# Optimization experiments

Hardware: AMD Instinct MI355X
Metric: run time of the kernel (lower is better)

## Reference

```python
import jax, jax.numpy as jnp
import numpy as np

B, S, E, H = 2, 2048, 1024, 16
HD = E // H


def setup_inputs() -> dict:
    key = jax.random.key(0)
    ks = jax.random.split(key, 5)
    scale = 1.0 / np.sqrt(E)
    return {
        "query": jax.random.normal(ks[0], (B, S, E), jnp.float32),
        "key": jax.random.normal(ks[1], (B, S, E), jnp.float32),
        "value": jax.random.normal(ks[2], (B, S, E), jnp.float32),
        "qkv_w": jax.random.normal(ks[3], (3 * E, E), jnp.float32) * scale,
        "qkv_b": jnp.zeros((3 * E,), jnp.float32),
        "out_w": jax.random.normal(ks[4], (E, E), jnp.float32) * scale,
        "out_b": jnp.zeros((E,), jnp.float32),
    }


def reference(query, key, value, qkv_w, qkv_b, out_w, out_b):
    # Fused QKV projection from query (module ignores key/value contents)
    qkv = query @ qkv_w.T + qkv_b                      # [B,S,3E]
    qkv = qkv.reshape(B, S, 3, H, HD)
    q = qkv[:, :, 0].transpose(0, 2, 1, 3)             # [B,H,S,HD]
    k = qkv[:, :, 1].transpose(0, 2, 1, 3)
    v = qkv[:, :, 2].transpose(0, 2, 1, 3)
    scaling = 1.0 / np.sqrt(HD)
    scores = jnp.einsum("bhqd,bhkd->bhqk", q, k) * scaling  # [B,H,S,S]
    probs = jax.nn.softmax(scores, axis=-1)
    ctx = jnp.einsum("bhqk,bhkd->bhqd", probs, v)      # [B,H,S,HD]
    ctx = ctx.transpose(0, 2, 1, 3).reshape(B, S, E)
    return ctx @ out_w.T + out_b
```

## Files before the change

### kernel.cpp

```cpp
#include <hip/hip_runtime.h>
#include <hip/hip_bf16.h>
#include <math.h>

#define BB 2
#define SS 2048
#define EE 1024
#define HH 16
#define HD 64

typedef __bf16 bf16;
typedef __bf16 bf16x8 __attribute__((ext_vector_type(8)));
typedef float floatx4 __attribute__((ext_vector_type(4)));
typedef float floatx16 __attribute__((ext_vector_type(16)));

#define MFMA(a, b, c) __builtin_amdgcn_mfma_f32_16x16x32_bf16(a, b, c, 0, 0, 0)
#define MFMA32(a, b, c) __builtin_amdgcn_mfma_f32_32x32x16_bf16(a, b, c, 0, 0, 0)

__device__ inline void async16(const bf16* g, bf16* l) {
    __builtin_amdgcn_global_load_lds(
        (const __attribute__((address_space(1))) void*)g,
        (__attribute__((address_space(3))) void*)l, 16, 0, 0);
}

__device__ inline unsigned cvt_pk_bf16(float a, float b) {
    unsigned r;
    asm("v_cvt_pk_bf16_f32 %0, %1, %2" : "=v"(r) : "v"(a), "v"(b));
    return r;
}

__global__ __launch_bounds__(256) void cvt3(
    const float* __restrict__ a, const float* __restrict__ b,
    const float* __restrict__ c,
    bf16* __restrict__ oa, bf16* __restrict__ ob, bf16* __restrict__ oc) {
    const long NA = (long)4096 * 1024, NB = (long)3072 * 1024, NC = (long)1024 * 1024;
    const long total = (NA + NB + NC) >> 2;
    long i = (long)blockIdx.x * blockDim.x + threadIdx.x;
    const long stride = (long)gridDim.x * blockDim.x;
    for (; i < total; i += stride) {
        const long e = i << 2;
        const float* src;
        bf16* dst;
        if (e < NA)           { src = a + e;            dst = oa + e; }
        else if (e < NA + NB) { src = b + (e - NA);     dst = ob + (e - NA); }
        else                  { src = c + (e - NA - NB); dst = oc + (e - NA - NB); }
        float4 v = *(const float4*)src;
        union { bf16 h[4]; uint2 u; } t;
        t.h[0] = (bf16)v.x; t.h[1] = (bf16)v.y; t.h[2] = (bf16)v.z; t.h[3] = (bf16)v.w;
        *(uint2*)dst = t.u;
    }
}

__global__ __launch_bounds__(256) void qkv_gemm(
    const bf16* __restrict__ A, const bf16* __restrict__ W,
    const float* __restrict__ bias,
    bf16* __restrict__ Qw, bf16* __restrict__ Kw, bf16* __restrict__ Vtw) {
    __shared__ __align__(16) bf16 As[128 * 64];
    __shared__ __align__(16) bf16 Bs[128 * 64];
    const int tid  = threadIdx.x;
    const int wave = tid >> 6, lane = tid & 63;
    const int quad = lane >> 4, l16 = lane & 15;
    const int wr = wave >> 1, wc = wave & 1;
    const int m0 = blockIdx.y * 128, n0 = blockIdx.x * 128;
    const int lr = lane >> 3;
    const int lc = (lane & 7) * 8;

    const bf16* Ag = A + (long)(m0 + wave * 32 + lr) * 1024 + lc;
    const bf16* Bg = W + (long)(n0 + wave * 32 + lr) * 1024 + lc;
    bf16* Al = As + (wave * 32) * 64 + lane * 8;
    bf16* Bl = Bs + (wave * 32) * 64 + lane * 8;

    floatx4 acc[4][4] = {};

    for (int k0 = 0; k0 < 1024; k0 += 64) {
        __syncthreads();
#pragma unroll
        for (int j = 0; j < 4; ++j) {
            async16(Ag + (long)j * 8 * 1024 + k0, Al + j * 8 * 64);
            async16(Bg + (long)j * 8 * 1024 + k0, Bl + j * 8 * 64);
        }
        __syncthreads();
#pragma unroll
        for (int c = 0; c < 2; ++c) {
            bf16x8 af[4], bfr[4];
#pragma unroll
            for (int mi = 0; mi < 4; ++mi)
                af[mi] = *(const bf16x8*)&As[(wr * 64 + mi * 16 + l16) * 64 + c * 32 + quad * 8];
#pragma unroll
            for (int ni = 0; ni < 4; ++ni)
                bfr[ni] = *(const bf16x8*)&Bs[(wc * 64 + ni * 16 + l16) * 64 + c * 32 + quad * 8];
#pragma unroll
            for (int mi = 0; mi < 4; ++mi)
#pragma unroll
                for (int ni = 0; ni < 4; ++ni)
                    acc[mi][ni] = MFMA(af[mi], bfr[ni], acc[mi][ni]);
        }
    }

#pragma unroll
    for (int mi = 0; mi < 4; ++mi)
#pragma unroll
        for (int ni = 0; ni < 4; ++ni) {
            const int n = n0 + wc * 64 + ni * 16 + l16;
            const float bn = bias[n];
            const int sel = n >> 10;
            const int e = n & 1023, h = e >> 6, d = e & 63;
            if (sel == 2) {
                const int m_base = m0 + wr * 64 + mi * 16 + quad * 4;
                const int b = m_base >> 11, s0 = m_base & 2047;
                union { bf16 h4[4]; uint2 u; } t;
#pragma unroll
                for (int r = 0; r < 4; ++r)
                    t.h4[r] = (bf16)(acc[mi][ni][r] + bn);
                *(uint2*)&Vtw[((long)(b * HH + h) * HD + d) * SS + s0] = t.u;
            } else {
#pragma unroll
                for (int r = 0; r < 4; ++r) {
                    const int m = m0 + wr * 64 + mi * 16 + quad * 4 + r;
                    const int b = m >> 11, s = m & 2047;
                    const float v = acc[mi][ni][r] + bn;
                    if (sel == 0)
                        Qw[((long)(b * HH + h) * SS + s) * HD + d] = (bf16)(v * 0.125f);
                    else
                        Kw[((long)(b * HH + h) * SS + s) * HD + d] = (bf16)v;
                }
            }
        }
}

__global__ __launch_bounds__(256) void attn(
    const bf16* __restrict__ Qw, const bf16* __restrict__ Kw,
    const bf16* __restrict__ Vtw, bf16* __restrict__ ctxw) {
    __shared__ __align__(16) bf16 Kt[64 * 64];
    __shared__ __align__(16) bf16 Vt[64 * 64];

    const int tid = threadIdx.x;
    const int wave = tid >> 6, lane = tid & 63;
    const int l5 = lane & 31, hi = lane >> 5;
    const int qb = blockIdx.x, bh = blockIdx.y;
    const bf16* Qh = Qw  + (long)bh * SS * HD;
    const bf16* Kh = Kw  + (long)bh * SS * HD;
    const bf16* Vh = Vtw + (long)bh * HD * SS;

    const int qbase = qb * 128 + wave * 32;
    bf16x8 qf[4];
#pragma unroll
    for (int d0 = 0; d0 < 4; ++d0)
        qf[d0] = *(const bf16x8*)&Qh[(long)(qbase + l5) * HD + d0 * 16 + hi * 8];

    floatx16 ctx0 = {}, ctx1 = {};
    float lsum = 0.f;

    const int srow = tid >> 2;
    const int sc0  = (tid & 3) * 16;
    const int swz  = (srow & 7) << 3;
    const int rswz = (l5 & 7) << 3;
    bf16* Kl0 = &Kt[srow * 64 + (sc0 ^ swz)];
    bf16* Kl1 = &Kt[srow * 64 + ((sc0 + 8) ^ swz)];
    bf16* Vl0 = &Vt[srow * 64 + (sc0 ^ swz)];
    bf16* Vl1 = &Vt[srow * 64 + ((sc0 + 8) ^ swz)];

    uint4 kr0, kr1, vr0, vr1;
    {
        const uint4* ks = (const uint4*)&Kh[(long)srow * HD + sc0];
        kr0 = ks[0]; kr1 = ks[1];
        const uint4* vs = (const uint4*)&Vh[(long)srow * SS + sc0];
        vr0 = vs[0]; vr1 = vs[1];
    }

    for (int kt = 0; kt < 32; ++kt) {
        __syncthreads();
        *(uint4*)Kl0 = kr0;
        *(uint4*)Kl1 = kr1;
        *(uint4*)Vl0 = vr0;
        *(uint4*)Vl1 = vr1;
        __syncthreads();

        if (kt < 31) {
            const uint4* ks = (const uint4*)&Kh[(long)((kt + 1) * 64 + srow) * HD + sc0];
            kr0 = ks[0]; kr1 = ks[1];
            const uint4* vs = (const uint4*)&Vh[(long)srow * SS + (kt + 1) * 64 + sc0];
            vr0 = vs[0]; vr1 = vs[1];
        }

        floatx16 sf[2];
#pragma unroll
        for (int kb = 0; kb < 2; ++kb) {
            floatx16 s = {};
#pragma unroll
            for (int d0 = 0; d0 < 4; ++d0) {
                const bf16x8 af = *(const bf16x8*)
                    &Kt[(kb * 32 + l5) * 64 + ((d0 * 16 + hi * 8) ^ rswz)];
                s = MFMA32(af, qf[d0], s);
            }
            sf[kb] = s;
        }

#pragma unroll
        for (int kb = 0; kb < 2; ++kb) {
#pragma unroll
            for (int r = 0; r < 16; ++r) {
                const float p = __expf(sf[kb][r]);
                sf[kb][r] = p;
                lsum += p;
            }
            unsigned w[8];
#pragma unroll
            for (int i = 0; i < 8; ++i)
                w[i] = cvt_pk_bf16(sf[kb][2 * i], sf[kb][2 * i + 1]);
            asm("v_permlane32_swap_b32 %0, %1" : "+v"(w[0]), "+v"(w[2]));
            asm("v_permlane32_swap_b32 %0, %1" : "+v"(w[1]), "+v"(w[3]));
            asm("v_permlane32_swap_b32 %0, %1" : "+v"(w[4]), "+v"(w[6]));
            asm("v_permlane32_swap_b32 %0, %1" : "+v"(w[5]), "+v"(w[7]));
            union { unsigned u[4]; bf16x8 v; } pa0 = {{w[0], w[1], w[2], w[3]}},
                                               pa1 = {{w[4], w[5], w[6], w[7]}};
#pragma unroll
            for (int kc = 0; kc < 2; ++kc) {
                const bf16x8 pa = kc ? pa1.v : pa0.v;
                const int kcol = kb * 32 + kc * 16 + hi * 8;
                const bf16x8 vf0 = *(const bf16x8*)&Vt[l5 * 64 + (kcol ^ rswz)];
                const bf16x8 vf1 = *(const bf16x8*)&Vt[(32 + l5) * 64 + (kcol ^ rswz)];
                ctx0 = MFMA32(pa, vf0, ctx0);
                ctx1 = MFMA32(pa, vf1, ctx1);
            }
        }
    }

    const float rs  = lsum + __shfl_xor(lsum, 32, 64);
    const float inv = 1.0f / rs;

    const int b = bh >> 4, h = bh & 15;
#pragma unroll
    for (int r = 0; r < 16; ++r) {
        const int qrow = (r & 3) + 8 * (r >> 2) + 4 * hi;
        const float iq = __shfl(inv, qrow, 64);
        const long base = ((long)b * SS + qbase + qrow) * EE + h * HD;
        ctxw[base + l5]      = (bf16)(ctx0[r] * iq);
        ctxw[base + 32 + l5] = (bf16)(ctx1[r] * iq);
    }
}

__global__ __launch_bounds__(256) void out_gemm(
    const bf16* __restrict__ A, const bf16* __restrict__ W,
    const float* __restrict__ bias, float* __restrict__ out) {
    __shared__ __align__(16) bf16 As[64 * 64];
    __shared__ __align__(16) bf16 Bs[128 * 64];
    const int tid  = threadIdx.x;
    const int wave = tid >> 6, lane = tid & 63;
    const int quad = lane >> 4, l16 = lane & 15;
    const int wr = wave & 1, wc = wave >> 1;
    const int m0 = blockIdx.y * 64, n0 = blockIdx.x * 128;
    const int lr = lane >> 3;
    const int lc = (lane & 7) * 8;

    const bf16* Ag = A + (long)(m0 + wave * 16 + lr) * 1024 + lc;
    const bf16* Bg = W + (long)(n0 + wave * 32 + lr) * 1024 + lc;
    bf16* Al = As + (wave * 16) * 64 + lane * 8;
    bf16* Bl = Bs + (wave * 32) * 64 + lane * 8;

    floatx4 acc[2][4] = {};

    for (int k0 = 0; k0 < 1024; k0 += 64) {
        __syncthreads();
#pragma unroll
        for (int j = 0; j < 2; ++j)
            async16(Ag + (long)j * 8 * 1024 + k0, Al + j * 8 * 64);
#pragma unroll
        for (int j = 0; j < 4; ++j)
            async16(Bg + (long)j * 8 * 1024 + k0, Bl + j * 8 * 64);
        __syncthreads();
#pragma unroll
        for (int c = 0; c < 2; ++c) {
            bf16x8 af[2], bfr[4];
#pragma unroll
            for (int mi = 0; mi < 2; ++mi)
                af[mi] = *(const bf16x8*)&As[(wr * 32 + mi * 16 + l16) * 64 + c * 32 + quad * 8];
#pragma unroll
            for (int ni = 0; ni < 4; ++ni)
                bfr[ni] = *(const bf16x8*)&Bs[(wc * 64 + ni * 16 + l16) * 64 + c * 32 + quad * 8];
#pragma unroll
            for (int mi = 0; mi < 2; ++mi)
#pragma unroll
                for (int ni = 0; ni < 4; ++ni)
                    acc[mi][ni] = MFMA(af[mi], bfr[ni], acc[mi][ni]);
        }
    }

#pragma unroll
    for (int mi = 0; mi < 2; ++mi)
#pragma unroll
        for (int ni = 0; ni < 4; ++ni) {
            const int n = n0 + wc * 64 + ni * 16 + l16;
            const float bn = bias[n];
#pragma unroll
            for (int r = 0; r < 4; ++r) {
                const int m = m0 + wr * 32 + mi * 16 + quad * 4 + r;
                out[(long)m * 1024 + n] = acc[mi][ni][r] + bn;
            }
        }
}

extern "C" void kernel_launch(void* const* d_in, const int* in_sizes, int n_in,
                              void* d_out, int out_size, void* d_ws, size_t ws_size,
                              hipStream_t stream) {
    const float* query = (const float*)d_in[0];
    const float* qkv_w = (const float*)d_in[3];
    const float* qkv_b = (const float*)d_in[4];
    const float* out_w = (const float*)d_in[5];
    const float* out_b = (const float*)d_in[6];

    const long NTOK = (long)BB * SS;
    bf16* qb   = (bf16*)d_ws;
    bf16* wqb  = qb  + NTOK * EE;
    bf16* owb  = wqb + (long)3 * EE * EE;
    bf16* Qw   = owb + (long)EE * EE;
    bf16* Kw   = Qw  + NTOK * EE;
    bf16* Vtw  = Kw  + NTOK * EE;
    bf16* ctxw = qb;
    float* out = (float*)d_out;

    cvt3<<<2048, 256, 0, stream>>>(query, qkv_w, out_w, qb, wqb, owb);
    qkv_gemm<<<dim3(24, 32), 256, 0, stream>>>(qb, wqb, qkv_b, Qw, Kw, Vtw);
    attn<<<dim3(16, 32), 256, 0, stream>>>(Qw, Kw, Vtw, ctxw);
    out_gemm<<<dim3(8, 64), 256, 0, stream>>>(ctxw, owb, out_b, out);
}
```

Before: 224.2 us.

## Double-buffer LDS tiles and XOR-swizzle layout in QKV and output GEMMs

Both projection GEMMs now keep two LDS buffers per operand. The async global-to-LDS copy of the next K-slice is issued before the MFMA work on the current slice, and the loop keeps one barrier per iteration instead of two. Each 16-byte chunk's column is XOR-swizzled with the row index on store and on fragment read, which is meant to cut LDS bank conflicts. The cost is twice the LDS per block, which may lower occupancy. The attention kernel is unchanged.

```diff
diff --git a/kernel.cpp b/kernel.cpp
--- a/kernel.cpp
+++ b/kernel.cpp
@@ -54,40 +54,49 @@
     const bf16* __restrict__ A, const bf16* __restrict__ W,
     const float* __restrict__ bias,
     bf16* __restrict__ Qw, bf16* __restrict__ Kw, bf16* __restrict__ Vtw) {
-    __shared__ __align__(16) bf16 As[128 * 64];
-    __shared__ __align__(16) bf16 Bs[128 * 64];
+    __shared__ __align__(16) bf16 As[2][128 * 64];
+    __shared__ __align__(16) bf16 Bs[2][128 * 64];
     const int tid  = threadIdx.x;
     const int wave = tid >> 6, lane = tid & 63;
     const int quad = lane >> 4, l16 = lane & 15;
     const int wr = wave >> 1, wc = wave & 1;
     const int m0 = blockIdx.y * 128, n0 = blockIdx.x * 128;
     const int lr = lane >> 3;
-    const int lc = (lane & 7) * 8;
-
-    const bf16* Ag = A + (long)(m0 + wave * 32 + lr) * 1024 + lc;
-    const bf16* Bg = W + (long)(n0 + wave * 32 + lr) * 1024 + lc;
-    bf16* Al = As + (wave * 32) * 64 + lane * 8;
-    bf16* Bl = Bs + (wave * 32) * 64 + lane * 8;
+    const int lcs = ((lane & 7) ^ (lr & 7)) * 8;
+    const int rsw = (l16 & 7) << 3;
+
+    const bf16* Ag = A + (long)(m0 + wave * 32 + lr) * 1024 + lcs;
+    const bf16* Bg = W + (long)(n0 + wave * 32 + lr) * 1024 + lcs;
+    const int lbase = (wave * 32) * 64 + lane * 8;
 
     floatx4 acc[4][4] = {};
 
-    for (int k0 = 0; k0 < 1024; k0 += 64) {
+#pragma unroll
+    for (int j = 0; j < 4; ++j) {
+        async16(Ag + (long)j * 8 * 1024, &As[0][lbase + j * 8 * 64]);
+        async16(Bg + (long)j * 8 * 1024, &Bs[0][lbase + j * 8 * 64]);
+    }
+
+    for (int ks = 0; ks < 16; ++ks) {
         __syncthreads();
-#pragma unroll
-        for (int j = 0; j < 4; ++j) {
-            async16(Ag + (long)j * 8 * 1024 + k0, Al + j * 8 * 64);
-            async16(Bg + (long)j * 8 * 1024 + k0, Bl + j * 8 * 64);
-        }
-        __syncthreads();
+        const int cur = ks & 1;
+        if (ks < 15) {
+            const int nxt = cur ^ 1, k0 = (ks + 1) * 64;
+#pragma unroll
+            for (int j = 0; j < 4; ++j) {
+                async16(Ag + (long)j * 8 * 1024 + k0, &As[nxt][lbase + j * 8 * 64]);
+                async16(Bg + (long)j * 8 * 1024 + k0, &Bs[nxt][lbase + j * 8 * 64]);
+            }
+        }
 #pragma unroll
         for (int c = 0; c < 2; ++c) {
             bf16x8 af[4], bfr[4];
 #pragma unroll
             for (int mi = 0; mi < 4; ++mi)
-                af[mi] = *(const bf16x8*)&As[(wr * 64 + mi * 16 + l16) * 64 + c * 32 + quad * 8];
+                af[mi] = *(const bf16x8*)&As[cur][(wr * 64 + mi * 16 + l16) * 64 + ((c * 32 + quad * 8) ^ rsw)];
 #pragma unroll
             for (int ni = 0; ni < 4; ++ni)
-                bfr[ni] = *(const bf16x8*)&Bs[(wc * 64 + ni * 16 + l16) * 64 + c * 32 + quad * 8];
+                bfr[ni] = *(const bf16x8*)&Bs[cur][(wc * 64 + ni * 16 + l16) * 64 + ((c * 32 + quad * 8) ^ rsw)];
 #pragma unroll
             for (int mi = 0; mi < 4; ++mi)
 #pragma unroll
@@ -242,41 +251,52 @@
 __global__ __launch_bounds__(256) void out_gemm(
     const bf16* __restrict__ A, const bf16* __restrict__ W,
     const float* __restrict__ bias, float* __restrict__ out) {
-    __shared__ __align__(16) bf16 As[64 * 64];
-    __shared__ __align__(16) bf16 Bs[128 * 64];
+    __shared__ __align__(16) bf16 As[2][64 * 64];
+    __shared__ __align__(16) bf16 Bs[2][128 * 64];
     const int tid  = threadIdx.x;
     const int wave = tid >> 6, lane = tid & 63;
     const int quad = lane >> 4, l16 = lane & 15;
     const int wr = wave & 1, wc = wave >> 1;
     const int m0 = blockIdx.y * 64, n0 = blockIdx.x * 128;
     const int lr = lane >> 3;
-    const int lc = (lane & 7) * 8;
-
-    const bf16* Ag = A + (long)(m0 + wave * 16 + lr) * 1024 + lc;
-    const bf16* Bg = W + (long)(n0 + wave * 32 + lr) * 1024 + lc;
-    bf16* Al = As + (wave * 16) * 64 + lane * 8;
-    bf16* Bl = Bs + (wave * 32) * 64 + lane * 8;
+    const int lcs = ((lane & 7) ^ (lr & 7)) * 8;
+    const int rsw = (l16 & 7) << 3;
+
+    const bf16* Ag = A + (long)(m0 + wave * 16 + lr) * 1024 + lcs;
+    const bf16* Bg = W + (long)(n0 + wave * 32 + lr) * 1024 + lcs;
+    const int labase = (wave * 16) * 64 + lane * 8;
+    const int lbbase = (wave * 32) * 64 + lane * 8;
 
     floatx4 acc[2][4] = {};
 
-    for (int k0 = 0; k0 < 1024; k0 += 64) {
+#pragma unroll
+    for (int j = 0; j < 2; ++j)
+        async16(Ag + (long)j * 8 * 1024, &As[0][labase + j * 8 * 64]);
+#pragma unroll
+    for (int j = 0; j < 4; ++j)
+        async16(Bg + (long)j * 8 * 1024, &Bs[0][lbbase + j * 8 * 64]);
+
+    for (int ks = 0; ks < 16; ++ks) {
         __syncthreads();
-#pragma unroll
-        for (int j = 0; j < 2; ++j)
-            async16(Ag + (long)j * 8 * 1024 + k0, Al + j * 8 * 64);
-#pragma unroll
-        for (int j = 0; j < 4; ++j)
-            async16(Bg + (long)j * 8 * 1024 + k0, Bl + j * 8 * 64);
-        __syncthreads();
+        const int cur = ks & 1;
+        if (ks < 15) {
+            const int nxt = cur ^ 1, k0 = (ks + 1) * 64;
+#pragma unroll
+            for (int j = 0; j < 2; ++j)
+                async16(Ag + (long)j * 8 * 1024 + k0, &As[nxt][labase + j * 8 * 64]);
+#pragma unroll
+            for (int j = 0; j < 4; ++j)
+                async16(Bg + (long)j * 8 * 1024 + k0, &Bs[nxt][lbbase + j * 8 * 64]);
+        }
 #pragma unroll
         for (int c = 0; c < 2; ++c) {
             bf16x8 af[2], bfr[4];
 #pragma unroll
             for (int mi = 0; mi < 2; ++mi)
-                af[mi] = *(const bf16x8*)&As[(wr * 32 + mi * 16 + l16) * 64 + c * 32 + quad * 8];
+                af[mi] = *(const bf16x8*)&As[cur][(wr * 32 + mi * 16 + l16) * 64 + ((c * 32 + quad * 8) ^ rsw)];
 #pragma unroll
             for (int ni = 0; ni < 4; ++ni)
-                bfr[ni] = *(const bf16x8*)&Bs[(wc * 64 + ni * 16 + l16) * 64 + c * 32 + quad * 8];
+                bfr[ni] = *(const bf16x8*)&Bs[cur][(wc * 64 + ni * 16 + l16) * 64 + ((c * 32 + quad * 8) ^ rsw)];
 #pragma unroll
             for (int mi = 0; mi < 2; ++mi)
 #pragma unroll
```

Result: faster. 219.1 us (-2.3%).
